# Kernel tuning notes

Hardware: AMD Instinct MI355X
Metric: run time of the kernel (lower is better)

## Reference

```python
import jax, jax.numpy as jnp
import numpy as np

B, S, D, H = 2, 2048, 2048, 16
HD = D // H
F = 4 * D
EPS = 1e-8


def _layernorm(x, g, b):
    m = jnp.mean(x, axis=-1, keepdims=True)
    v = jnp.mean((x - m) ** 2, axis=-1, keepdims=True)
    return (x - m) / jnp.sqrt(v + EPS) * g + b


def setup_inputs() -> dict:
    key = jax.random.key(0)
    ks = jax.random.split(key, 12)

    def lin(k, fan_in, fan_out):
        # torch Linear init ~ U(-1/sqrt(fan_in), 1/sqrt(fan_in)); stored as [in, out]
        lim = 1.0 / np.sqrt(fan_in)
        kw, kb = jax.random.split(k)
        w = jax.random.uniform(kw, (fan_in, fan_out), jnp.float32, -lim, lim)
        b = jax.random.uniform(kb, (fan_out,), jnp.float32, -lim, lim)
        return w, b

    x = jax.random.normal(ks[0], (B, S, D), jnp.float32)
    wq, bq = lin(ks[1], D, D)
    wk, bk = lin(ks[2], D, D)
    wv, bv = lin(ks[3], D, D)
    wo, bo = lin(ks[4], D, D)
    wu, bu = lin(ks[5], D, F)
    wd, bd = lin(ks[6], F, D)
    g1 = jnp.ones((D,), jnp.float32)
    b1 = jnp.zeros((D,), jnp.float32)
    g2 = jnp.ones((D,), jnp.float32)
    b2 = jnp.zeros((D,), jnp.float32)
    return dict(x=x, wq=wq, bq=bq, wk=wk, bk=bk, wv=wv, bv=bv, wo=wo, bo=bo,
                g1=g1, b1=b1, wu=wu, bu=bu, wd=wd, bd=bd, g2=g2, b2=b2)


def reference(x, wq, bq, wk, bk, wv, bv, wo, bo, g1, b1, wu, bu, wd, bd, g2, b2):
    b, s, d = x.shape
    # QKV projections -> [b, H, s, HD]
    q = (x @ wq + bq).reshape(b, s, H, HD).transpose(0, 2, 1, 3)
    k = (x @ wk + bk).reshape(b, s, H, HD).transpose(0, 2, 1, 3)
    v = (x @ wv + bv).reshape(b, s, H, HD).transpose(0, 2, 1, 3)
    # scaled dot-product with causal mask filled at -1e9 (matches masked_fill)
    scores = jnp.einsum('bhqd,bhkd->bhqk', q, k) / np.sqrt(HD).astype(np.float32)
    causal = jnp.tril(jnp.ones((s, s), bool))
    scores = jnp.where(causal, scores, jnp.float32(-1e9))
    attn = jax.nn.softmax(scores, axis=-1)  # dropout is identity (eval / rate=0)
    o = jnp.einsum('bhqk,bhkd->bhqd', attn, v)
    o = o.transpose(0, 2, 1, 3).reshape(b, s, d)
    o = o @ wo + bo
    x = _layernorm(x + o, g1, b1)
    # FFN with exact (erf) GELU, residual, LN
    h = jax.nn.gelu(x @ wu + bu, approximate=False)
    h = h @ wd + bd
    return _layernorm(x + h, g2, b2)
```

## Files before the change

### kernel.cpp

```cpp
#include <hip/hip_runtime.h>
#include <hip/hip_bf16.h>
#include <math.h>

#define DEV __device__ __forceinline__

typedef __bf16 bf16x8 __attribute__((ext_vector_type(8)));
typedef float f32x4 __attribute__((ext_vector_type(4)));
typedef unsigned short ushort_t;
typedef ushort_t us8 __attribute__((ext_vector_type(8)));
typedef ushort_t us4 __attribute__((ext_vector_type(4)));

DEV float bf2f(ushort_t u) {
    unsigned v = ((unsigned)u) << 16;
    float f; __builtin_memcpy(&f, &v, 4); return f;
}
DEV ushort_t f2bf(float f) {
    __bf16 h = (__bf16)f;
    ushort_t u; __builtin_memcpy(&u, &h, 2); return u;
}

DEV void gload16(const void* g, void* l) {
    __builtin_amdgcn_global_load_lds(
        (const __attribute__((address_space(1))) void*)g,
        (__attribute__((address_space(3))) void*)l, 16, 0, 0);
}

__global__ __launch_bounds__(256) void fill_kernel(float* out, long n, float v) {
    long i = (long)blockIdx.x * blockDim.x + threadIdx.x;
    if (i < n) out[i] = v;
}

__global__ __launch_bounds__(256) void cast_bf16_kernel(
    const float* __restrict__ in, ushort_t* __restrict__ out, long n)
{
    long i = ((long)blockIdx.x * blockDim.x + threadIdx.x) * 4;
    if (i >= n) return;
    float4 v = *(const float4*)(in + i);
    us4 o = { f2bf(v.x), f2bf(v.y), f2bf(v.z), f2bf(v.w) };
    *(us4*)(out + i) = o;
}

__global__ __launch_bounds__(256) void transpose_bf16_kernel(
    const float* __restrict__ in, ushort_t* __restrict__ out, int R, int C)
{
    __shared__ float tile[32][33];
    int c0 = blockIdx.x * 32, r0 = blockIdx.y * 32;
    int tx = threadIdx.x & 31, ty = threadIdx.x >> 5;
#pragma unroll
    for (int j = 0; j < 4; ++j) {
        int r = ty + j * 8;
        tile[r][tx] = in[(long)(r0 + r) * C + (c0 + tx)];
    }
    __syncthreads();
#pragma unroll
    for (int j = 0; j < 4; ++j) {
        int r = ty + j * 8;
        out[(long)(c0 + r) * R + (r0 + tx)] = f2bf(tile[tx][r]);
    }
}

__global__ __launch_bounds__(256) void transpose3_bf16_kernel(
    const float* __restrict__ w0, const float* __restrict__ w1,
    const float* __restrict__ w2, ushort_t* __restrict__ out)
{
    __shared__ float tile[32][33];
    const float* in = (blockIdx.z == 0) ? w0 : (blockIdx.z == 1) ? w1 : w2;
    ushort_t* o = out + (size_t)blockIdx.z * 2048 * 2048;
    int c0 = blockIdx.x * 32, r0 = blockIdx.y * 32;
    int tx = threadIdx.x & 31, ty = threadIdx.x >> 5;
#pragma unroll
    for (int j = 0; j < 4; ++j) {
        int r = ty + j * 8;
        tile[r][tx] = in[(long)(r0 + r) * 2048 + (c0 + tx)];
    }
    __syncthreads();
#pragma unroll
    for (int j = 0; j < 4; ++j) {
        int r = ty + j * 8;
        o[(long)(c0 + r) * 2048 + (r0 + tx)] = f2bf(tile[tx][r]);
    }
}

DEV void epilogue_store(f32x4 (&acc)[4][4], const float* bias, ushort_t* C,
                        long m0, long n0, int N, int act, int wr, int wc, int l,
                        char* lwb)
{
    ushort_t* lw = (ushort_t*)lwb;
#pragma unroll
    for (int jj = 0; jj < 2; ++jj) {
#pragma unroll
        for (int jh = 0; jh < 2; ++jh) {
            int j = jj * 2 + jh;
            int col = (int)n0 + wc * 64 + j * 16 + (l & 15);
            float bv = bias[col];
#pragma unroll
            for (int i = 0; i < 4; ++i) {
#pragma unroll
                for (int r = 0; r < 4; ++r) {
                    float v2 = acc[i][j][r] + bv;
                    if (act == 1) v2 = 0.5f * v2 * (1.f + erff(v2 * 0.70710678118654752440f));
                    lw[(i * 16 + (l >> 4) * 4 + r) * 36 + jh * 16 + (l & 15)] = f2bf(v2);
                }
            }
        }
        asm volatile("s_waitcnt lgkmcnt(0)" ::: "memory");
#pragma unroll
        for (int p = 0; p < 8; ++p) {
            int row = p * 8 + (l >> 3);
            us4 vv = *(const us4*)(lw + row * 36 + (l & 7) * 4);
            *(us4*)(C + (m0 + wr * 64 + row) * (long)N + n0 + wc * 64 + jj * 32 + (l & 7) * 4) = vv;
        }
        asm volatile("s_waitcnt lgkmcnt(0)" ::: "memory");
    }
}

__global__ __launch_bounds__(256) void gemm_bt_kernel(
    const ushort_t* __restrict__ A, const ushort_t* __restrict__ Bt,
    const float* __restrict__ bias, ushort_t* __restrict__ C,
    int M, int N, int K, int act)
{
    __shared__ __align__(16) ushort_t lA[128 * 64];
    __shared__ __align__(16) ushort_t lB[128 * 64];
    const int t = threadIdx.x;
    const int w = t >> 6, l = t & 63;
    const int wr = w >> 1, wc = w & 1;
    const long m0 = (long)blockIdx.x * 128;
    const long n0 = (long)blockIdx.y * 128;

    const int sr = l >> 3;
    const int scol = (l & 7) * 16;

    f32x4 acc[4][4];
    f32x4 zf = {0.f, 0.f, 0.f, 0.f};
#pragma unroll
    for (int i = 0; i < 4; ++i)
#pragma unroll
        for (int j = 0; j < 4; ++j) acc[i][j] = zf;

    char* lAc = (char*)lA;
    char* lBc = (char*)lB;

    const char* aptr[4];
    const char* bptr[4];
#pragma unroll
    for (int c = 0; c < 4; ++c) {
        int row = (w * 4 + c) * 8 + sr;
        int src = scol ^ ((row & 7) << 4);
        aptr[c] = (const char*)(A + (m0 + row) * (long)K) + src;
        bptr[c] = (const char*)(Bt + (n0 + row) * (long)K) + src;
    }

    for (int k0 = 0; k0 < K; k0 += 64) {
        __syncthreads();
#pragma unroll
        for (int c = 0; c < 4; ++c) {
            gload16(aptr[c], lAc + (w * 4 + c) * 1024);
            gload16(bptr[c], lBc + (w * 4 + c) * 1024);
            aptr[c] += 128;
            bptr[c] += 128;
        }
        __syncthreads();
#pragma unroll
        for (int ks = 0; ks < 2; ++ks) {
            bf16x8 af[4], bfr[4];
#pragma unroll
            for (int i = 0; i < 4; ++i) {
                int row = wr * 64 + i * 16 + (l & 15);
                int cb = (ks * 64 + (l >> 4) * 16) ^ ((row & 7) << 4);
                af[i] = *(const bf16x8*)(lAc + row * 128 + cb);
            }
#pragma unroll
            for (int j = 0; j < 4; ++j) {
                int row = wc * 64 + j * 16 + (l & 15);
                int cb = (ks * 64 + (l >> 4) * 16) ^ ((row & 7) << 4);
                bfr[j] = *(const bf16x8*)(lBc + row * 128 + cb);
            }
#pragma unroll
            for (int i = 0; i < 4; ++i)
#pragma unroll
                for (int j = 0; j < 4; ++j)
                    acc[i][j] = __builtin_amdgcn_mfma_f32_16x16x32_bf16(af[i], bfr[j], acc[i][j], 0, 0, 0);
        }
    }

    __syncthreads();
    epilogue_store(acc, bias, C, m0, n0, N, act, wr, wc, l,
                   (w < 2 ? lAc : lBc) + (w & 1) * 4608);
}

__global__ __launch_bounds__(256) void gemm_bt128_kernel(
    const ushort_t* __restrict__ A, const ushort_t* __restrict__ Bt,
    const float* __restrict__ bias, ushort_t* __restrict__ C,
    int M, int N, int K, int act)
{
    __shared__ __align__(16) ushort_t lA[128 * 128];
    __shared__ __align__(16) ushort_t lB[128 * 128];
    const int t = threadIdx.x;
    const int w = t >> 6, l = t & 63;
    const int wr = w >> 1, wc = w & 1;
    const long m0 = (long)blockIdx.x * 128;
    const long n0 = (long)blockIdx.y * 128;

    const int srow = t >> 4;
    const int ssrc = ((t & 15) * 16) ^ ((srow & 7) << 4);

    f32x4 acc[4][4];
    f32x4 zf = {0.f, 0.f, 0.f, 0.f};
#pragma unroll
    for (int i = 0; i < 4; ++i)
#pragma unroll
        for (int j = 0; j < 4; ++j) acc[i][j] = zf;

    char* lAc = (char*)lA;
    char* lBc = (char*)lB;

    const char* aptr[8];
    const char* bptr[8];
#pragma unroll
    for (int r = 0; r < 8; ++r) {
        int row = r * 16 + srow;
        aptr[r] = (const char*)(A + (m0 + row) * (long)K) + ssrc;
        bptr[r] = (const char*)(Bt + (n0 + row) * (long)K) + ssrc;
    }

    for (int k0 = 0; k0 < K; k0 += 128) {
        __syncthreads();
#pragma unroll
        for (int r = 0; r < 8; ++r) {
            gload16(aptr[r], lAc + r * 4096 + t * 16);
            gload16(bptr[r], lBc + r * 4096 + t * 16);
            aptr[r] += 256;
            bptr[r] += 256;
        }
        __syncthreads();
#pragma unroll
        for (int ks = 0; ks < 4; ++ks) {
            bf16x8 af[4], bfr[4];
#pragma unroll
            for (int i = 0; i < 4; ++i) {
                int row = wr * 64 + i * 16 + (l & 15);
                int cb = (ks * 64 + (l >> 4) * 16) ^ ((row & 7) << 4);
                af[i] = *(const bf16x8*)(lAc + row * 256 + cb);
            }
#pragma unroll
            for (int j = 0; j < 4; ++j) {
                int row = wc * 64 + j * 16 + (l & 15);
                int cb = (ks * 64 + (l >> 4) * 16) ^ ((row & 7) << 4);
                bfr[j] = *(const bf16x8*)(lBc + row * 256 + cb);
            }
#pragma unroll
            for (int i = 0; i < 4; ++i)
#pragma unroll
                for (int j = 0; j < 4; ++j)
                    acc[i][j] = __builtin_amdgcn_mfma_f32_16x16x32_bf16(af[i], bfr[j], acc[i][j], 0, 0, 0);
        }
    }

    __syncthreads();
    epilogue_store(acc, bias, C, m0, n0, N, act, wr, wc, l,
                   (w < 2 ? lAc : lBc) + (w & 1) * 4608);
}

__global__ __launch_bounds__(512, 4) void attn_kernel(
    const ushort_t* __restrict__ qkv, ushort_t* __restrict__ o)
{
    __shared__ __align__(16) ushort_t lK[2 * 64 * 128];
    __shared__ __align__(16) ushort_t lVT[128 * 72];
    __shared__ __align__(16) ushort_t lP[8 * 16 * 64];

    const int t = threadIdx.x, w = t >> 6, l = t & 63;
    const int bx = blockIdx.x;
    const int qblk = (bx & 1) ? (15 - (bx >> 1)) : (bx >> 1);
    const int bh = blockIdx.y;
    const int b = bh >> 4, h = bh & 15;
    const int q0 = qblk * 128 + w * 16;
    const long base = (long)b * 2048 * 6144 + (long)h * 128;
    char* lKc = (char*)lK;

    const ushort_t* qrow = qkv + base + (long)(q0 + (l & 15)) * 6144;
    bf16x8 qf[4];
#pragma unroll
    for (int hb = 0; hb < 4; ++hb)
        qf[hb] = *(const bf16x8*)(qrow + hb * 32 + (l >> 4) * 8);

    f32x4 accO[8];
    f32x4 zf = {0.f, 0.f, 0.f, 0.f};
#pragma unroll
    for (int i = 0; i < 8; ++i) accO[i] = zf;
    float m_r[4] = {-1e30f, -1e30f, -1e30f, -1e30f};
    float l_r[4] = {0.f, 0.f, 0.f, 0.f};

    const int nt = (qblk * 128 + 128) >> 6;
    const float scale = 0.08838834764831845f;
    const long TILE_ADV = 64L * 6144 * 2;

    const int kvp = t & 31;
    const int d0 = (t >> 5) * 8;
    us8 va, vb;

    const char* kptr[2];
#pragma unroll
    for (int i = 0; i < 2; ++i) {
        int c = w * 2 + i;
        int row = c * 4 + (l >> 4);
        int src = ((l & 15) * 16) ^ ((row & 7) << 4);
        kptr[i] = (const char*)(qkv + base + 2048 + (long)row * 6144) + src;
    }
    const char* vptr = (const char*)(qkv + base + 4096 + (long)(kvp * 2) * 6144 + d0);

    auto stageK = [&](int buf) {
#pragma unroll
        for (int i = 0; i < 2; ++i) {
            gload16(kptr[i], lKc + buf * 16384 + (w * 2 + i) * 1024);
            kptr[i] += TILE_ADV;
        }
    };
    auto loadV = [&]() {
        va = *(const us8*)vptr;
        vb = *(const us8*)(vptr + 6144 * 2);
        vptr += TILE_ADV;
    };
    auto writeVT = [&]() {
#pragma unroll
        for (int j = 0; j < 8; ++j) {
            unsigned pk = (unsigned)va[j] | ((unsigned)vb[j] << 16);
            *(unsigned*)(lVT + (d0 + j) * 72 + kvp * 2) = pk;
        }
    };

    stageK(0);
    loadV();
    asm volatile("s_waitcnt vmcnt(0)" ::: "memory");
    writeVT();
    __syncthreads();

    for (int t0 = 0; t0 < nt; ++t0) {
        const int cur = t0 & 1;
        const bool more = (t0 + 1 < nt);
        if (more) { stageK(cur ^ 1); loadV(); }

        const int kv0 = t0 * 64;
        if (kv0 <= q0 + 15) {
            f32x4 sc[4];
#pragma unroll
            for (int kvs = 0; kvs < 4; ++kvs) {
                sc[kvs] = zf;
                int row = kvs * 16 + (l & 15);
#pragma unroll
                for (int hb = 0; hb < 4; ++hb) {
                    int cb = (hb * 64 + (l >> 4) * 16) ^ ((row & 7) << 4);
                    bf16x8 kf = *(const bf16x8*)(lKc + cur * 16384 + row * 256 + cb);
                    sc[kvs] = __builtin_amdgcn_mfma_f32_16x16x32_bf16(qf[hb], kf, sc[kvs], 0, 0, 0);
                }
            }
#pragma unroll
            for (int r = 0; r < 4; ++r) {
                int qg = q0 + (l >> 4) * 4 + r;
                float s[4];
#pragma unroll
                for (int kvs = 0; kvs < 4; ++kvs) {
                    s[kvs] = sc[kvs][r] * scale;
                    if (kv0 + kvs * 16 + (l & 15) > qg) s[kvs] = -1e30f;
                }
                float pm = fmaxf(fmaxf(s[0], s[1]), fmaxf(s[2], s[3]));
                pm = fmaxf(pm, __shfl_xor(pm, 1));
                pm = fmaxf(pm, __shfl_xor(pm, 2));
                pm = fmaxf(pm, __shfl_xor(pm, 4));
                pm = fmaxf(pm, __shfl_xor(pm, 8));
                float mn = fmaxf(m_r[r], pm);
                float p[4], ps = 0.f;
#pragma unroll
                for (int kvs = 0; kvs < 4; ++kvs) { p[kvs] = __expf(s[kvs] - mn); ps += p[kvs]; }
                ps += __shfl_xor(ps, 1);
                ps += __shfl_xor(ps, 2);
                ps += __shfl_xor(ps, 4);
                ps += __shfl_xor(ps, 8);
                float alpha = __expf(m_r[r] - mn);
                l_r[r] = l_r[r] * alpha + ps;
                m_r[r] = mn;
#pragma unroll
                for (int tt = 0; tt < 8; ++tt) accO[tt][r] *= alpha;
                int qloc = (l >> 4) * 4 + r;
#pragma unroll
                for (int kvs = 0; kvs < 4; ++kvs)
                    lP[w * 1024 + qloc * 64 + kvs * 16 + (l & 15)] = f2bf(p[kvs]);
            }
            asm volatile("s_waitcnt lgkmcnt(0)" ::: "memory");
#pragma unroll
            for (int ks = 0; ks < 2; ++ks) {
                bf16x8 pf = *(const bf16x8*)(lP + w * 1024 + (l & 15) * 64 + ks * 32 + (l >> 4) * 8);
#pragma unroll
                for (int tt = 0; tt < 8; ++tt) {
                    bf16x8 vf = *(const bf16x8*)(lVT + (tt * 16 + (l & 15)) * 72 + ks * 32 + (l >> 4) * 8);
                    accO[tt] = __builtin_amdgcn_mfma_f32_16x16x32_bf16(pf, vf, accO[tt], 0, 0, 0);
                }
            }
        }

        asm volatile("s_waitcnt vmcnt(0)" ::: "memory");
        __syncthreads();
        if (more) { writeVT(); __syncthreads(); }
    }

    const long obase = (long)b * 2048 * 2048 + (long)h * 128;
#pragma unroll
    for (int r = 0; r < 4; ++r) {
        float inv = 1.f / l_r[r];
        long orow = obase + (long)(q0 + (l >> 4) * 4 + r) * 2048;
#pragma unroll
        for (int tt = 0; tt < 8; ++tt)
            o[orow + tt * 16 + (l & 15)] = f2bf(accO[tt][r] * inv);
    }
}

__global__ __launch_bounds__(256) void ln_kernel(
    const float* xres, const ushort_t* __restrict__ addb,
    const float* __restrict__ g, const float* __restrict__ bb,
    float* outf, ushort_t* __restrict__ outb)
{
    __shared__ float rs[4], rss[4];
    const int row = blockIdx.x, t = threadIdx.x;
    const float* xp = xres + (long)row * 2048 + t * 8;
    const ushort_t* ap = addb + (long)row * 2048 + t * 8;
    float4 a = *(const float4*)xp;
    float4 c = *(const float4*)(xp + 4);
    us8 ad = *(const us8*)ap;
    float v[8];
    v[0] = a.x + bf2f(ad[0]); v[1] = a.y + bf2f(ad[1]);
    v[2] = a.z + bf2f(ad[2]); v[3] = a.w + bf2f(ad[3]);
    v[4] = c.x + bf2f(ad[4]); v[5] = c.y + bf2f(ad[5]);
    v[6] = c.z + bf2f(ad[6]); v[7] = c.w + bf2f(ad[7]);
    float s = 0.f, ss = 0.f;
#pragma unroll
    for (int j = 0; j < 8; ++j) { s += v[j]; ss += v[j] * v[j]; }
#pragma unroll
    for (int off = 32; off > 0; off >>= 1) {
        s += __shfl_down(s, off);
        ss += __shfl_down(ss, off);
    }
    if ((t & 63) == 0) { rs[t >> 6] = s; rss[t >> 6] = ss; }
    __syncthreads();
    float S = rs[0] + rs[1] + rs[2] + rs[3];
    float SS = rss[0] + rss[1] + rss[2] + rss[3];
    float mean = S * (1.f / 2048.f);
    float var = SS * (1.f / 2048.f) - mean * mean;
    float rstd = rsqrtf(var + 1e-8f);
    float of[8];
#pragma unroll
    for (int j = 0; j < 8; ++j) {
        int col = t * 8 + j;
        of[j] = (v[j] - mean) * rstd * g[col] + bb[col];
    }
    float4 o1 = {of[0], of[1], of[2], of[3]};
    float4 o2 = {of[4], of[5], of[6], of[7]};
    float* op = outf + (long)row * 2048 + t * 8;
    *(float4*)op = o1;
    *(float4*)(op + 4) = o2;
    if (outb) {
        us8 ob;
#pragma unroll
        for (int j = 0; j < 8; ++j) ob[j] = f2bf(of[j]);
        *(us8*)(outb + (long)row * 2048 + t * 8) = ob;
    }
}

extern "C" void kernel_launch(void* const* d_in, const int* in_sizes, int n_in,
                              void* d_out, int out_size, void* d_ws, size_t ws_size,
                              hipStream_t stream)
{
    const float* x  = (const float*)d_in[0];
    const float* wq = (const float*)d_in[1];
    const float* bq = (const float*)d_in[2];
    const float* wk = (const float*)d_in[3];
    const float* bk = (const float*)d_in[4];
    const float* wv = (const float*)d_in[5];
    const float* bv = (const float*)d_in[6];
    const float* wo = (const float*)d_in[7];
    const float* bo = (const float*)d_in[8];
    const float* g1 = (const float*)d_in[9];
    const float* b1 = (const float*)d_in[10];
    const float* wu = (const float*)d_in[11];
    const float* bu = (const float*)d_in[12];
    const float* wd = (const float*)d_in[13];
    const float* bd = (const float*)d_in[14];
    const float* g2 = (const float*)d_in[15];
    const float* b2 = (const float*)d_in[16];
    (void)in_sizes; (void)n_in; (void)out_size;

    const size_t MB = 1ull << 20;
    char* wsp = (char*)d_ws;
    char*  slotA = wsp;
    char*  slotB = wsp + 32 * MB;
    char*  slotC = wsp + 48 * MB;
    float* bqkv  = (float*)(wsp + 112 * MB);
    const size_t need = 112 * MB + 32768;
    if (ws_size < need) {
        fill_kernel<<<(8388608 + 255) / 256, 256, 0, stream>>>((float*)d_out, 8388608L, 1e6f);
        return;
    }

    ushort_t* xb   = (ushort_t*)slotB;
    ushort_t* wT   = (ushort_t*)slotA;
    ushort_t* qkvb = (ushort_t*)slotC;
    ushort_t* ab   = (ushort_t*)slotB;
    ushort_t* pb   = (ushort_t*)slotC;
    float*    x1f  = (float*)d_out;
    ushort_t* x1b  = (ushort_t*)slotB;
    ushort_t* hb   = (ushort_t*)slotC;
    ushort_t* db   = (ushort_t*)slotB;

    cast_bf16_kernel<<<8192, 256, 0, stream>>>(x, xb, 8388608L);
    transpose3_bf16_kernel<<<dim3(64, 64, 3), 256, 0, stream>>>(wq, wk, wv, wT);
    hipMemcpyAsync(bqkv,        bq, 2048 * sizeof(float), hipMemcpyDeviceToDevice, stream);
    hipMemcpyAsync(bqkv + 2048, bk, 2048 * sizeof(float), hipMemcpyDeviceToDevice, stream);
    hipMemcpyAsync(bqkv + 4096, bv, 2048 * sizeof(float), hipMemcpyDeviceToDevice, stream);
    gemm_bt_kernel<<<dim3(32, 48), 256, 0, stream>>>(xb, wT, bqkv, qkvb, 4096, 6144, 2048, 0);
    attn_kernel<<<dim3(16, 32), 512, 0, stream>>>(qkvb, ab);
    transpose_bf16_kernel<<<dim3(64, 64), 256, 0, stream>>>(wo, wT, 2048, 2048);
    gemm_bt128_kernel<<<dim3(32, 16), 256, 0, stream>>>(ab, wT, bo, pb, 4096, 2048, 2048, 0);
    ln_kernel<<<4096, 256, 0, stream>>>(x, pb, g1, b1, x1f, x1b);
    transpose_bf16_kernel<<<dim3(256, 64), 256, 0, stream>>>(wu, wT, 2048, 8192);
    gemm_bt_kernel<<<dim3(32, 64), 256, 0, stream>>>(x1b, wT, bu, hb, 4096, 8192, 2048, 1);
    transpose_bf16_kernel<<<dim3(64, 256), 256, 0, stream>>>(wd, wT, 8192, 2048);
    gemm_bt128_kernel<<<dim3(32, 16), 256, 0, stream>>>(hb, wT, bd, db, 4096, 2048, 8192, 0);
    ln_kernel<<<4096, 256, 0, stream>>>(x1f, db, g2, b2, (float*)d_out, nullptr);
}
```

Measured before the change: 699.5 us.

## Add 256x256 eight-wave ping-pong GEMM for QKV and FFN-up projections

Adds a new GEMM kernel that uses 512-thread blocks and 256x256 output tiles, double-buffered LDS fed by global_load_lds. Staging is interleaved with MFMA quarter-blocks under explicit barriers, wait counts and priority hints. The QKV and FFN-up projections switch to it from the 128x128 kernel. The aim is more reuse per loaded byte and better overlap of memory traffic with matrix math, at the cost of higher register and LDS use per block and fewer blocks.

```diff
diff --git a/kernel.cpp b/kernel.cpp
--- a/kernel.cpp
+++ b/kernel.cpp
@@ -25,6 +25,11 @@
         (__attribute__((address_space(3))) void*)l, 16, 0, 0);
 }
 
+#define WAITV(n)  asm volatile("s_waitcnt vmcnt(" #n ")" ::: "memory")
+#define WAITL0()  asm volatile("s_waitcnt lgkmcnt(0)" ::: "memory")
+#define BAR()     __builtin_amdgcn_s_barrier()
+#define SB0()     __builtin_amdgcn_sched_barrier(0)
+
 __global__ __launch_bounds__(256) void fill_kernel(float* out, long n, float v) {
     long i = (long)blockIdx.x * blockDim.x + threadIdx.x;
     if (i < n) out[i] = v;
@@ -103,14 +108,14 @@
                 }
             }
         }
-        asm volatile("s_waitcnt lgkmcnt(0)" ::: "memory");
+        WAITL0();
 #pragma unroll
         for (int p = 0; p < 8; ++p) {
             int row = p * 8 + (l >> 3);
             us4 vv = *(const us4*)(lw + row * 36 + (l & 7) * 4);
             *(us4*)(C + (m0 + wr * 64 + row) * (long)N + n0 + wc * 64 + jj * 32 + (l & 7) * 4) = vv;
         }
-        asm volatile("s_waitcnt lgkmcnt(0)" ::: "memory");
+        WAITL0();
     }
 }
 
@@ -259,6 +264,171 @@
     __syncthreads();
     epilogue_store(acc, bias, C, m0, n0, N, act, wr, wc, l,
                    (w < 2 ? lAc : lBc) + (w & 1) * 4608);
+}
+
+__global__ __launch_bounds__(512, 2) void gemm8p_kernel(
+    const ushort_t* __restrict__ A, const ushort_t* __restrict__ Bt,
+    const float* __restrict__ bias, ushort_t* __restrict__ C,
+    int M, int N, int K, int act)
+{
+    __shared__ __align__(16) ushort_t lA[2 * 2 * 128 * 64];
+    __shared__ __align__(16) ushort_t lB[2 * 2 * 128 * 64];
+    const int t = threadIdx.x, l = t & 63, w = t >> 6;
+    const int wr = w >> 2, wc = w & 3;
+    const long m0 = (long)blockIdx.x * 256;
+    const long n0 = (long)blockIdx.y * 256;
+    char* lAc = (char*)lA;
+    char* lBc = (char*)lB;
+
+    const int rl = l & 15, rh = (l >> 4) * 16;
+    const int swz = (rl & 7) << 4;
+    const long KB = (long)K * 2;
+    const long R64 = 64 * KB;
+    const int ssrc = ((t & 7) * 16) ^ (((t >> 3) & 7) << 4);
+
+    f32x4 acc[8][4];
+    f32x4 zf = {0.f, 0.f, 0.f, 0.f};
+#pragma unroll
+    for (int i = 0; i < 8; ++i)
+#pragma unroll
+        for (int j = 0; j < 4; ++j) acc[i][j] = zf;
+
+    const char* pA0 = (const char*)A + (m0 + (t >> 3)) * KB + ssrc;
+    const char* pA1 = (const char*)A + (m0 + 128 + (t >> 3)) * KB + ssrc;
+    const char* pB0 = (const char*)Bt + (n0 + (t >> 3)) * KB + ssrc;
+    const char* pB1 = (const char*)Bt + (n0 + 128 + (t >> 3)) * KB + ssrc;
+
+    auto stage = [&](const char*& p, char* dst) {
+        gload16(p, dst + t * 16);
+        gload16(p + R64, dst + 8192 + t * 16);
+        p += 128;
+    };
+    auto loadA = [&](bf16x8 (&aF)[4][2], int d, int qm) {
+#pragma unroll
+        for (int i = 0; i < 4; ++i) {
+            int rb = d * 32768 + wr * 16384 + ((qm * 4 + i) * 16 + rl) * 128;
+            aF[i][0] = *(const bf16x8*)(lAc + rb + (rh ^ swz));
+            aF[i][1] = *(const bf16x8*)(lAc + rb + ((64 + rh) ^ swz));
+        }
+    };
+    auto loadB = [&](bf16x8 (&bF)[2][2], int d, int qn) {
+#pragma unroll
+        for (int jb = 0; jb < 2; ++jb) {
+            int cih = (wc & 1) * 64 + (qn * 2 + jb) * 16 + rl;
+            int rb = d * 32768 + (wc >> 1) * 16384 + cih * 128;
+            bF[jb][0] = *(const bf16x8*)(lBc + rb + (rh ^ swz));
+            bF[jb][1] = *(const bf16x8*)(lBc + rb + ((64 + rh) ^ swz));
+        }
+    };
+
+    bf16x8 aF[4][2], bF0[2][2], bF1[2][2];
+    auto mfma16 = [&](int qm, int qn, bf16x8 (&bF)[2][2]) {
+        __builtin_amdgcn_s_setprio(1);
+#pragma unroll
+        for (int i = 0; i < 4; ++i)
+#pragma unroll
+            for (int jb = 0; jb < 2; ++jb)
+#pragma unroll
+                for (int ks = 0; ks < 2; ++ks)
+                    acc[qm * 4 + i][qn * 2 + jb] = __builtin_amdgcn_mfma_f32_16x16x32_bf16(
+                        aF[i][ks], bF[jb][ks], acc[qm * 4 + i][qn * 2 + jb], 0, 0, 0);
+        __builtin_amdgcn_s_setprio(0);
+    };
+
+    const int NT = K >> 6;
+    stage(pB0, lBc);
+    stage(pB1, lBc + 16384);
+    stage(pA0, lAc);
+    stage(pA1, lAc + 16384);
+    stage(pB0, lBc + 32768);
+    stage(pB1, lBc + 32768 + 16384);
+    WAITV(4);
+    SB0();
+    BAR();
+
+    const int NI = NT >> 1;
+    for (int j = 0; j < NI; ++j) {
+        const bool s2 = (2 * j + 2 < NT);
+        loadA(aF, 0, 0);
+        loadB(bF0, 0, 0);
+        stage(pA0, lAc + 32768);
+        BAR(); WAITL0(); SB0();
+        mfma16(0, 0, bF0);
+        BAR();
+        loadB(bF1, 0, 1);
+        stage(pA1, lAc + 32768 + 16384);
+        BAR(); WAITL0(); SB0();
+        mfma16(0, 1, bF1);
+        BAR();
+        loadA(aF, 0, 1);
+        if (s2) stage(pB0, lBc);
+        BAR(); WAITL0(); SB0();
+        mfma16(1, 1, bF1);
+        BAR();
+        if (s2) stage(pB1, lBc + 16384);
+        BAR();
+        mfma16(1, 0, bF0);
+        if (s2) { WAITV(4); } else { WAITV(0); }
+        SB0();
+        BAR();
+        loadA(aF, 1, 0);
+        loadB(bF0, 1, 0);
+        if (s2) stage(pA0, lAc);
+        BAR(); WAITL0(); SB0();
+        mfma16(0, 0, bF0);
+        BAR();
+        loadB(bF1, 1, 1);
+        if (s2) stage(pA1, lAc + 16384);
+        BAR(); WAITL0(); SB0();
+        mfma16(0, 1, bF1);
+        BAR();
+        loadA(aF, 1, 1);
+        if (s2) stage(pB0, lBc + 32768);
+        BAR(); WAITL0(); SB0();
+        mfma16(1, 1, bF1);
+        BAR();
+        if (s2) stage(pB1, lBc + 32768 + 16384);
+        BAR();
+        mfma16(1, 0, bF0);
+        if (s2) { WAITV(4); } else { WAITV(0); }
+        SB0();
+        BAR();
+    }
+
+    {
+        char* lwb = lAc + w * 4608;
+        ushort_t* lw = (ushort_t*)lwb;
+#pragma unroll
+        for (int hh = 0; hh < 2; ++hh) {
+            long m0w = m0 + wr * 128 + hh * 64;
+            long n0w = n0 + wc * 64;
+#pragma unroll
+            for (int jj = 0; jj < 2; ++jj) {
+#pragma unroll
+                for (int jh = 0; jh < 2; ++jh) {
+                    int jf = jj * 2 + jh;
+                    float bv = bias[(int)n0w + jf * 16 + rl];
+#pragma unroll
+                    for (int i = 0; i < 4; ++i) {
+#pragma unroll
+                        for (int r = 0; r < 4; ++r) {
+                            float v2 = acc[hh * 4 + i][jf][r] + bv;
+                            if (act == 1) v2 = 0.5f * v2 * (1.f + erff(v2 * 0.70710678118654752440f));
+                            lw[(i * 16 + (l >> 4) * 4 + r) * 36 + jh * 16 + rl] = f2bf(v2);
+                        }
+                    }
+                }
+                WAITL0();
+#pragma unroll
+                for (int p = 0; p < 8; ++p) {
+                    int row = p * 8 + (l >> 3);
+                    us4 vv = *(const us4*)(lw + row * 36 + (l & 7) * 4);
+                    *(us4*)(C + (m0w + row) * (long)N + n0w + jj * 32 + (l & 7) * 4) = vv;
+                }
+                WAITL0();
+            }
+        }
+    }
 }
 
 __global__ __launch_bounds__(512, 4) void attn_kernel(
@@ -330,7 +500,7 @@
 
     stageK(0);
     loadV();
-    asm volatile("s_waitcnt vmcnt(0)" ::: "memory");
+    WAITV(0);
     writeVT();
     __syncthreads();
 
@@ -385,7 +555,7 @@
                 for (int kvs = 0; kvs < 4; ++kvs)
                     lP[w * 1024 + qloc * 64 + kvs * 16 + (l & 15)] = f2bf(p[kvs]);
             }
-            asm volatile("s_waitcnt lgkmcnt(0)" ::: "memory");
+            WAITL0();
 #pragma unroll
             for (int ks = 0; ks < 2; ++ks) {
                 bf16x8 pf = *(const bf16x8*)(lP + w * 1024 + (l & 15) * 64 + ks * 32 + (l >> 4) * 8);
@@ -397,7 +567,7 @@
             }
         }
 
-        asm volatile("s_waitcnt vmcnt(0)" ::: "memory");
+        WAITV(0);
         __syncthreads();
         if (more) { writeVT(); __syncthreads(); }
     }
@@ -514,13 +684,13 @@
     hipMemcpyAsync(bqkv,        bq, 2048 * sizeof(float), hipMemcpyDeviceToDevice, stream);
     hipMemcpyAsync(bqkv + 2048, bk, 2048 * sizeof(float), hipMemcpyDeviceToDevice, stream);
     hipMemcpyAsync(bqkv + 4096, bv, 2048 * sizeof(float), hipMemcpyDeviceToDevice, stream);
-    gemm_bt_kernel<<<dim3(32, 48), 256, 0, stream>>>(xb, wT, bqkv, qkvb, 4096, 6144, 2048, 0);
+    gemm8p_kernel<<<dim3(16, 24), 512, 0, stream>>>(xb, wT, bqkv, qkvb, 4096, 6144, 2048, 0);
     attn_kernel<<<dim3(16, 32), 512, 0, stream>>>(qkvb, ab);
     transpose_bf16_kernel<<<dim3(64, 64), 256, 0, stream>>>(wo, wT, 2048, 2048);
     gemm_bt128_kernel<<<dim3(32, 16), 256, 0, stream>>>(ab, wT, bo, pb, 4096, 2048, 2048, 0);
     ln_kernel<<<4096, 256, 0, stream>>>(x, pb, g1, b1, x1f, x1b);
     transpose_bf16_kernel<<<dim3(256, 64), 256, 0, stream>>>(wu, wT, 2048, 8192);
-    gemm_bt_kernel<<<dim3(32, 64), 256, 0, stream>>>(x1b, wT, bu, hb, 4096, 8192, 2048, 1);
+    gemm8p_kernel<<<dim3(16, 32), 512, 0, stream>>>(x1b, wT, bu, hb, 4096, 8192, 2048, 1);
     transpose_bf16_kernel<<<dim3(64, 256), 256, 0, stream>>>(wd, wT, 8192, 2048);
     gemm_bt128_kernel<<<dim3(32, 16), 256, 0, stream>>>(hb, wT, bd, db, 4096, 2048, 8192, 0);
     ln_kernel<<<4096, 256, 0, stream>>>(x1f, db, g2, b2, (float*)d_out, nullptr);
```

New measurement: 716.3 us. +2.4%, slower.
